# Performance work log

Measured on AMD Instinct MI355X. Metric: run time of the kernel, lower is better.

## Reference

```python
import jax, jax.numpy as jnp
import numpy as np

N = 50000   # nodes
E = 600000  # edges
D = 128     # in_feats
H = 128     # n_hidden
C = 47      # n_classes


def setup_inputs() -> dict:
    key = jax.random.key(0)
    ks = jax.random.split(key, 12)
    x = jax.random.normal(ks[0], (N, D), dtype=jnp.float32)
    src = jax.random.randint(ks[1], (E,), 0, N, dtype=jnp.int32)
    dst = jax.random.randint(ks[2], (E,), 0, N, dtype=jnp.int32)
    def lin(k, fi, fo):
        s = 1.0 / np.sqrt(fi)
        return jax.random.uniform(k, (fi, fo), jnp.float32, -s, s)
    return {
        "x": x, "src": src, "dst": dst,
        "W_self0": lin(ks[3], D, H), "W_neigh0": lin(ks[4], D, H), "b0": jnp.zeros((H,), jnp.float32),
        "W_self1": lin(ks[5], H, H), "W_neigh1": lin(ks[6], H, H), "b1": jnp.zeros((H,), jnp.float32),
        "W_self2": lin(ks[7], H, C), "W_neigh2": lin(ks[8], H, C), "b2": jnp.zeros((C,), jnp.float32),
    }


def _sage_layer(h, src, dst, W_self, W_neigh, b, act):
    # gather neighbor (src) features, mean-aggregate onto dst nodes
    msum = jax.ops.segment_sum(h[src], dst, num_segments=N)           # [N, F]
    deg = jax.ops.segment_sum(jnp.ones((src.shape[0], 1), h.dtype), dst, num_segments=N)
    h_neigh = msum / jnp.maximum(deg, 1.0)                            # zero-degree -> 0
    out = h @ W_self + h_neigh @ W_neigh + b
    return jax.nn.relu(out) if act else out


def reference(x, src, dst, W_self0, W_neigh0, b0, W_self1, W_neigh1, b1, W_self2, W_neigh2, b2):
    h = _sage_layer(x, src, dst, W_self0, W_neigh0, b0, True)
    h = _sage_layer(h, src, dst, W_self1, W_neigh1, b1, True)
    h = _sage_layer(h, src, dst, W_self2, W_neigh2, b2, False)
    return h
```

## Files before the change

kernel.cpp:

```cpp
#include <hip/hip_runtime.h>
#include <hip/hip_bf16.h>


#define THREADS 256

typedef unsigned short u16;
typedef __attribute__((ext_vector_type(8))) short bf16x8;
typedef __attribute__((ext_vector_type(4))) float f32x4;

__device__ inline u16 f2bf(float f) {
    union { float f; unsigned u; } v; v.f = f;
    unsigned r = (v.u + 0x7FFFu + ((v.u >> 16) & 1u)) >> 16;
    return (u16)r;
}
__device__ inline float bf2f(u16 b) {
    union { unsigned u; float f; } v; v.u = ((unsigned)b) << 16;
    return v.f;
}
__device__ inline unsigned pack2(float a, float b) {
    return (unsigned)f2bf(a) | ((unsigned)f2bf(b) << 16);
}

#define GLDS16(gp, lp)                                                         \
    __builtin_amdgcn_global_load_lds(                                          \
        (const __attribute__((address_space(1))) void*)(gp),                   \
        (__attribute__((address_space(3))) void*)(lp), 16, 0, 0)

__global__ void k_prepcount(const int* __restrict__ dst, int* __restrict__ deg, int E,
                            const float* __restrict__ x, u16* __restrict__ hi,
                            u16* __restrict__ lo, int n32,
                            const float* __restrict__ Ws0, const float* __restrict__ Wn0,
                            const float* __restrict__ Ws1, const float* __restrict__ Wn1,
                            const float* __restrict__ Ws2, const float* __restrict__ Wn2,
                            u16* __restrict__ Bt) {
    int idx = blockIdx.x * blockDim.x + threadIdx.x;
    if (idx < E) {
        atomicAdd(&deg[dst[idx]], 1);
        return;
    }
    idx -= E;
    if (idx < n32) {
        float4 v = ((const float4*)x)[idx];
        float h0 = bf2f(f2bf(v.x)), h1 = bf2f(f2bf(v.y));
        float h2 = bf2f(f2bf(v.z)), h3 = bf2f(f2bf(v.w));
        uint2 hp, lp;
        hp.x = pack2(h0, h1); hp.y = pack2(h2, h3);
        lp.x = pack2(v.x - h0, v.y - h1); lp.y = pack2(v.z - h2, v.w - h3);
        ((uint2*)hi)[idx] = hp;
        ((uint2*)lo)[idx] = lp;
        return;
    }
    idx -= n32;
    if (idx < 3 * 128 * 256) {
        int layer = idx >> 15;
        int within = idx & 32767;
        int col = within >> 8;
        int k = within & 255;
        const float* Ws = (layer == 0) ? Ws0 : (layer == 1) ? Ws1 : Ws2;
        const float* Wn = (layer == 0) ? Wn0 : (layer == 1) ? Wn1 : Wn2;
        int fo = (layer == 2) ? 47 : 128;
        float v = 0.f;
        if (col < fo) v = (k < 128) ? Ws[k * fo + col] : Wn[(k - 128) * fo + col];
        u16 h = f2bf(v);
        Bt[layer * 65536 + within] = h;
        Bt[layer * 65536 + 32768 + within] = f2bf(v - bf2f(h));
    }
}

__global__ void k_scan_block(const int* __restrict__ deg, int* __restrict__ off,
                             int* __restrict__ bsum, int n) {
    __shared__ int s[256];
    int t = threadIdx.x;
    int base = blockIdx.x * 1024 + t * 4;
    int v[4];
#pragma unroll
    for (int i = 0; i < 4; i++) v[i] = (base + i < n) ? deg[base + i] : 0;
    int sum = v[0] + v[1] + v[2] + v[3];
    int val = sum;
    s[t] = val;
    __syncthreads();
    for (int o = 1; o < 256; o <<= 1) {
        int x = (t >= o) ? s[t - o] : 0;
        __syncthreads();
        val += x;
        s[t] = val;
        __syncthreads();
    }
    int run = val - sum;
#pragma unroll
    for (int i = 0; i < 4; i++) {
        if (base + i < n) off[base + i] = run;
        run += v[i];
    }
    if (t == 255) bsum[blockIdx.x] = val;
}

__global__ void k_scan_bsum(int* __restrict__ bsum, int nb) {
    int lane = threadIdx.x;
    int carry = 0;
    for (int start = 0; start < nb; start += 64) {
        int i = start + lane;
        int orig = (i < nb) ? bsum[i] : 0;
        int v = orig;
#pragma unroll
        for (int o = 1; o < 64; o <<= 1) {
            int u = __shfl_up(v, o, 64);
            if (lane >= o) v += u;
        }
        if (i < nb) bsum[i] = carry + v - orig;
        carry += __shfl(v, 63, 64);
    }
}

__global__ void k_scan_add(int* __restrict__ off, const int* __restrict__ bsum, int n) {
    int t = threadIdx.x;
    int base = blockIdx.x * 1024 + t * 4;
    int add = bsum[blockIdx.x];
#pragma unroll
    for (int i = 0; i < 4; i++)
        if (base + i < n) off[base + i] += add;
}

__global__ void k_fill(const int* __restrict__ src, const int* __restrict__ dst,
                       const int* __restrict__ off, int* __restrict__ cur,
                       int* __restrict__ eidx, int E) {
    int e = blockIdx.x * blockDim.x + threadIdx.x;
    if (e < E) {
        int d = dst[e];
        int p = atomicAdd(&cur[d], 1);
        eidx[off[d] + p] = src[e];
    }
}

__global__ void k_aggregate(const u16* __restrict__ hi_in, const int* __restrict__ eidx,
                            const int* __restrict__ off, const int* __restrict__ deg,
                            u16* __restrict__ mhi, u16* __restrict__ mlo, int n) {
    int wv = blockIdx.x * 4 + (threadIdx.x >> 6);
    int lane = threadIdx.x & 63;
    int half = lane >> 5;
    int hl = lane & 31;
    int node = wv * 2 + half;
    if (node >= n) return;
    int cnt = deg[node];
    int base = off[node];
    const uint2* h2 = (const uint2*)hi_in;
    float4 acc = make_float4(0.f, 0.f, 0.f, 0.f);
    for (int j = 0; j < cnt; j += 8) {
        int s[8];
        float m[8];
#pragma unroll
        for (int u = 0; u < 8; u++) {
            int jj = j + u;
            s[u] = eidx[base + (jj < cnt ? jj : 0)];
            m[u] = (jj < cnt) ? 1.f : 0.f;
        }
        uint2 v[8];
#pragma unroll
        for (int u = 0; u < 8; u++) v[u] = h2[(size_t)s[u] * 32 + hl];
#pragma unroll
        for (int u = 0; u < 8; u++) {
            acc.x = fmaf(m[u], bf2f((u16)(v[u].x & 0xffffu)), acc.x);
            acc.y = fmaf(m[u], bf2f((u16)(v[u].x >> 16)), acc.y);
            acc.z = fmaf(m[u], bf2f((u16)(v[u].y & 0xffffu)), acc.z);
            acc.w = fmaf(m[u], bf2f((u16)(v[u].y >> 16)), acc.w);
        }
    }
    float iv = 1.0f / (float)(cnt > 1 ? cnt : 1);
    float a0 = acc.x * iv, a1 = acc.y * iv, a2 = acc.z * iv, a3 = acc.w * iv;
    float r0 = bf2f(f2bf(a0)), r1 = bf2f(f2bf(a1)), r2 = bf2f(f2bf(a2)), r3 = bf2f(f2bf(a3));
    uint2 hp, lp;
    hp.x = pack2(a0, a1); hp.y = pack2(a2, a3);
    lp.x = pack2(a0 - r0, a1 - r1); lp.y = pack2(a2 - r2, a3 - r3);
    ((uint2*)mhi)[(size_t)node * 32 + hl] = hp;
    ((uint2*)mlo)[(size_t)node * 32 + hl] = lp;
}

__global__ __launch_bounds__(256) void k_gemm_mfma(
    const u16* __restrict__ Ahi_s, const u16* __restrict__ Alo_s,
    const u16* __restrict__ Ahi_n, const u16* __restrict__ Alo_n,
    const u16* __restrict__ Bthi, const u16* __restrict__ Btlo,
    const float* __restrict__ bias, float* __restrict__ out_f32,
    u16* __restrict__ out_hi, u16* __restrict__ out_lo, int n, int fout, int relu) {
    __shared__ u16 sAhi[128 * 32];
    __shared__ u16 sAlo[128 * 32];
    __shared__ u16 sBhi[128 * 32];
    __shared__ u16 sBlo[128 * 32];

    int t = threadIdx.x;
    int w = t >> 6;
    int lane = t & 63;
    int wr = w >> 1, wc = w & 1;
    size_t row0 = (size_t)blockIdx.x * 128;

    f32x4 acc[4][4];
#pragma unroll
    for (int r = 0; r < 4; r++)
#pragma unroll
        for (int c = 0; c < 4; c++) acc[r][c] = (f32x4){0.f, 0.f, 0.f, 0.f};

    for (int kk = 0; kk < 256; kk += 32) {
        const u16* Phi = (kk < 128) ? Ahi_s : Ahi_n;
        const u16* Plo = (kk < 128) ? Alo_s : Alo_n;
        int kc = kk & 127;
        __syncthreads();
#pragma unroll
        for (int i = 0; i < 2; i++) {
            int r = w * 32 + i * 16 + (lane >> 2);
            int cb = (lane & 3) * 8;
            GLDS16(Phi + (row0 + r) * 128 + kc + cb, &sAhi[r * 32 + cb]);
            GLDS16(Plo + (row0 + r) * 128 + kc + cb, &sAlo[r * 32 + cb]);
        }
#pragma unroll
        for (int i = 0; i < 2; i++) {
            int c = w * 32 + i * 16 + (lane >> 2);
            int cb = (lane & 3) * 8;
            GLDS16(Bthi + (size_t)c * 256 + kk + cb, &sBhi[c * 32 + cb]);
            GLDS16(Btlo + (size_t)c * 256 + kk + cb, &sBlo[c * 32 + cb]);
        }
        __syncthreads();

        bf16x8 a_hi[4], a_lo[4], b_hi[4], b_lo[4];
        int q8 = (lane >> 4) * 8;
#pragma unroll
        for (int r = 0; r < 4; r++) {
            int ad = (wr * 64 + r * 16 + (lane & 15)) * 32 + q8;
            a_hi[r] = *(const bf16x8*)&sAhi[ad];
            a_lo[r] = *(const bf16x8*)&sAlo[ad];
        }
#pragma unroll
        for (int c = 0; c < 4; c++) {
            int ad = (wc * 64 + c * 16 + (lane & 15)) * 32 + q8;
            b_hi[c] = *(const bf16x8*)&sBhi[ad];
            b_lo[c] = *(const bf16x8*)&sBlo[ad];
        }
#pragma unroll
        for (int r = 0; r < 4; r++)
#pragma unroll
            for (int c = 0; c < 4; c++) {
                acc[r][c] = __builtin_amdgcn_mfma_f32_16x16x32_bf16(
                    a_hi[r], b_hi[c], acc[r][c], 0, 0, 0);
                acc[r][c] = __builtin_amdgcn_mfma_f32_16x16x32_bf16(
                    a_hi[r], b_lo[c], acc[r][c], 0, 0, 0);
                acc[r][c] = __builtin_amdgcn_mfma_f32_16x16x32_bf16(
                    a_lo[r], b_hi[c], acc[r][c], 0, 0, 0);
            }
    }

    int quad = lane >> 4;
    int lcol = lane & 15;
#pragma unroll
    for (int r = 0; r < 4; r++) {
#pragma unroll
        for (int c = 0; c < 4; c++) {
            int col = wc * 64 + c * 16 + lcol;
            float bv = (col < fout) ? bias[col] : 0.f;
#pragma unroll
            for (int g = 0; g < 4; g++) {
                size_t row = row0 + wr * 64 + r * 16 + quad * 4 + g;
                if (row >= (size_t)n || col >= fout) continue;
                float v = acc[r][c][g] + bv;
                if (relu) v = v > 0.f ? v : 0.f;
                if (out_f32) out_f32[row * fout + col] = v;
                if (out_hi) {
                    u16 h = f2bf(v);
                    out_hi[row * 128 + col] = h;
                    out_lo[row * 128 + col] = f2bf(v - bf2f(h));
                }
            }
        }
    }
}

extern "C" void kernel_launch(void* const* d_in, const int* in_sizes, int n_in,
                              void* d_out, int out_size, void* d_ws, size_t ws_size,
                              hipStream_t stream) {
    const float* x = (const float*)d_in[0];
    const int* src = (const int*)d_in[1];
    const int* dst = (const int*)d_in[2];
    const float* Ws0 = (const float*)d_in[3];
    const float* Wn0 = (const float*)d_in[4];
    const float* b0 = (const float*)d_in[5];
    const float* Ws1 = (const float*)d_in[6];
    const float* Wn1 = (const float*)d_in[7];
    const float* b1 = (const float*)d_in[8];
    const float* Ws2 = (const float*)d_in[9];
    const float* Wn2 = (const float*)d_in[10];
    const float* b2 = (const float*)d_in[11];
    float* out = (float*)d_out;

    const int N = in_sizes[0] / 128;
    const int E = in_sizes[1];
    const int Npad = ((N + 127) / 128) * 128;

    char* p = (char*)d_ws;
    u16* P0hi = (u16*)p; p += (size_t)Npad * 128 * 2;
    u16* P0lo = (u16*)p; p += (size_t)Npad * 128 * 2;
    u16* P1hi = (u16*)p; p += (size_t)Npad * 128 * 2;
    u16* P1lo = (u16*)p; p += (size_t)Npad * 128 * 2;
    u16* Mhi = (u16*)p; p += (size_t)Npad * 128 * 2;
    u16* Mlo = (u16*)p; p += (size_t)Npad * 128 * 2;
    u16* Bt = (u16*)p; p += 3 * 2 * 128 * 256 * 2;
    int* deg = (int*)p; p += (size_t)N * 4;
    int* cur = (int*)p; p += (size_t)N * 4;
    int* off = (int*)p; p += (size_t)N * 4;
    int* eidx = (int*)p; p += (size_t)E * 4;
    int* bsum = (int*)p;

    const int nbE = (E + THREADS - 1) / THREADS;
    const int nbScan = (N + 1023) / 1024;
    const int nbAgg = (N + 7) / 8;
    const int nbGemm = Npad / 128;
    const int prepTotal = E + N * 32 + 3 * 128 * 256;
    const int nbPrep = (prepTotal + THREADS - 1) / THREADS;

    hipMemsetAsync(deg, 0, (size_t)2 * N * sizeof(int), stream);

    k_prepcount<<<nbPrep, THREADS, 0, stream>>>(dst, deg, E, x, P0hi, P0lo, N * 32,
                                                Ws0, Wn0, Ws1, Wn1, Ws2, Wn2, Bt);
    k_scan_block<<<nbScan, 256, 0, stream>>>(deg, off, bsum, N);
    k_scan_bsum<<<1, 64, 0, stream>>>(bsum, nbScan);
    k_scan_add<<<nbScan, 256, 0, stream>>>(off, bsum, N);
    k_fill<<<nbE, THREADS, 0, stream>>>(src, dst, off, cur, eidx, E);

    k_aggregate<<<nbAgg, 256, 0, stream>>>(P0hi, eidx, off, deg, Mhi, Mlo, N);
    k_gemm_mfma<<<nbGemm, 256, 0, stream>>>(P0hi, P0lo, Mhi, Mlo,
                                            Bt + 0 * 65536, Bt + 0 * 65536 + 32768, b0,
                                            (float*)nullptr, P1hi, P1lo, N, 128, 1);
    k_aggregate<<<nbAgg, 256, 0, stream>>>(P1hi, eidx, off, deg, Mhi, Mlo, N);
    k_gemm_mfma<<<nbGemm, 256, 0, stream>>>(P1hi, P1lo, Mhi, Mlo,
                                            Bt + 1 * 65536, Bt + 1 * 65536 + 32768, b1,
                                            (float*)nullptr, P0hi, P0lo, N, 128, 1);
    k_aggregate<<<nbAgg, 256, 0, stream>>>(P0hi, eidx, off, deg, Mhi, Mlo, N);
    k_gemm_mfma<<<nbGemm, 256, 0, stream>>>(P0hi, P0lo, Mhi, Mlo,
                                            Bt + 2 * 65536, Bt + 2 * 65536 + 32768, b2,
                                            out, (u16*)nullptr, (u16*)nullptr, N, 47, 0);
}
```

Measured before the change: 317.1 us.

## Load GEMM operands directly from global into registers with smaller 64-row tiles

The MFMA GEMM no longer stages A and B tiles through shared memory with global_load_lds and barriers. Each wave now loads its bf16x8 fragments straight from global memory. The row tile shrinks from 128 to 64, which doubles the number of blocks and halves the accumulators per wave. This removes LDS traffic and synchronisation and raises parallelism, at the cost of redundant global/L2 reads of B and A across waves with no shared reuse.

```diff
diff --git a/kernel.cpp b/kernel.cpp
--- a/kernel.cpp
+++ b/kernel.cpp
@@ -20,11 +20,6 @@
 __device__ inline unsigned pack2(float a, float b) {
     return (unsigned)f2bf(a) | ((unsigned)f2bf(b) << 16);
 }
-
-#define GLDS16(gp, lp)                                                         \
-    __builtin_amdgcn_global_load_lds(                                          \
-        (const __attribute__((address_space(1))) void*)(gp),                   \
-        (__attribute__((address_space(3))) void*)(lp), 16, 0, 0)
 
 __global__ void k_prepcount(const int* __restrict__ dst, int* __restrict__ deg, int E,
                             const float* __restrict__ x, u16* __restrict__ hi,
@@ -181,60 +176,41 @@
     const u16* __restrict__ Bthi, const u16* __restrict__ Btlo,
     const float* __restrict__ bias, float* __restrict__ out_f32,
     u16* __restrict__ out_hi, u16* __restrict__ out_lo, int n, int fout, int relu) {
-    __shared__ u16 sAhi[128 * 32];
-    __shared__ u16 sAlo[128 * 32];
-    __shared__ u16 sBhi[128 * 32];
-    __shared__ u16 sBlo[128 * 32];
-
     int t = threadIdx.x;
     int w = t >> 6;
     int lane = t & 63;
     int wr = w >> 1, wc = w & 1;
-    size_t row0 = (size_t)blockIdx.x * 128;
-
-    f32x4 acc[4][4];
-#pragma unroll
-    for (int r = 0; r < 4; r++)
+    int m16 = lane & 15;
+    int q8 = (lane >> 4) * 8;
+    size_t row0 = (size_t)blockIdx.x * 64;
+
+    f32x4 acc[2][4];
+#pragma unroll
+    for (int r = 0; r < 2; r++)
 #pragma unroll
         for (int c = 0; c < 4; c++) acc[r][c] = (f32x4){0.f, 0.f, 0.f, 0.f};
 
+#pragma unroll
     for (int kk = 0; kk < 256; kk += 32) {
         const u16* Phi = (kk < 128) ? Ahi_s : Ahi_n;
         const u16* Plo = (kk < 128) ? Alo_s : Alo_n;
-        int kc = kk & 127;
-        __syncthreads();
-#pragma unroll
-        for (int i = 0; i < 2; i++) {
-            int r = w * 32 + i * 16 + (lane >> 2);
-            int cb = (lane & 3) * 8;
-            GLDS16(Phi + (row0 + r) * 128 + kc + cb, &sAhi[r * 32 + cb]);
-            GLDS16(Plo + (row0 + r) * 128 + kc + cb, &sAlo[r * 32 + cb]);
-        }
-#pragma unroll
-        for (int i = 0; i < 2; i++) {
-            int c = w * 32 + i * 16 + (lane >> 2);
-            int cb = (lane & 3) * 8;
-            GLDS16(Bthi + (size_t)c * 256 + kk + cb, &sBhi[c * 32 + cb]);
-            GLDS16(Btlo + (size_t)c * 256 + kk + cb, &sBlo[c * 32 + cb]);
-        }
-        __syncthreads();
-
-        bf16x8 a_hi[4], a_lo[4], b_hi[4], b_lo[4];
-        int q8 = (lane >> 4) * 8;
-#pragma unroll
-        for (int r = 0; r < 4; r++) {
-            int ad = (wr * 64 + r * 16 + (lane & 15)) * 32 + q8;
-            a_hi[r] = *(const bf16x8*)&sAhi[ad];
-            a_lo[r] = *(const bf16x8*)&sAlo[ad];
+        int kc = (kk & 127) + q8;
+
+        bf16x8 a_hi[2], a_lo[2], b_hi[4], b_lo[4];
+#pragma unroll
+        for (int r = 0; r < 2; r++) {
+            size_t ra = (row0 + wr * 32 + r * 16 + m16) * 128 + kc;
+            a_hi[r] = *(const bf16x8*)(Phi + ra);
+            a_lo[r] = *(const bf16x8*)(Plo + ra);
         }
 #pragma unroll
         for (int c = 0; c < 4; c++) {
-            int ad = (wc * 64 + c * 16 + (lane & 15)) * 32 + q8;
-            b_hi[c] = *(const bf16x8*)&sBhi[ad];
-            b_lo[c] = *(const bf16x8*)&sBlo[ad];
-        }
-#pragma unroll
-        for (int r = 0; r < 4; r++)
+            size_t ba = (size_t)(wc * 64 + c * 16 + m16) * 256 + kk + q8;
+            b_hi[c] = *(const bf16x8*)(Bthi + ba);
+            b_lo[c] = *(const bf16x8*)(Btlo + ba);
+        }
+#pragma unroll
+        for (int r = 0; r < 2; r++)
 #pragma unroll
             for (int c = 0; c < 4; c++) {
                 acc[r][c] = __builtin_amdgcn_mfma_f32_16x16x32_bf16(
@@ -249,14 +225,14 @@
     int quad = lane >> 4;
     int lcol = lane & 15;
 #pragma unroll
-    for (int r = 0; r < 4; r++) {
+    for (int r = 0; r < 2; r++) {
 #pragma unroll
         for (int c = 0; c < 4; c++) {
             int col = wc * 64 + c * 16 + lcol;
             float bv = (col < fout) ? bias[col] : 0.f;
 #pragma unroll
             for (int g = 0; g < 4; g++) {
-                size_t row = row0 + wr * 64 + r * 16 + quad * 4 + g;
+                size_t row = row0 + wr * 32 + r * 16 + quad * 4 + g;
                 if (row >= (size_t)n || col >= fout) continue;
                 float v = acc[r][c][g] + bv;
                 if (relu) v = v > 0.f ? v : 0.f;
@@ -290,7 +266,7 @@
 
     const int N = in_sizes[0] / 128;
     const int E = in_sizes[1];
-    const int Npad = ((N + 127) / 128) * 128;
+    const int Npad = ((N + 63) / 64) * 64;
 
     char* p = (char*)d_ws;
     u16* P0hi = (u16*)p; p += (size_t)Npad * 128 * 2;
@@ -309,7 +285,7 @@
     const int nbE = (E + THREADS - 1) / THREADS;
     const int nbScan = (N + 1023) / 1024;
     const int nbAgg = (N + 7) / 8;
-    const int nbGemm = Npad / 128;
+    const int nbGemm = Npad / 64;
     const int prepTotal = E + N * 32 + 3 * 128 * 256;
     const int nbPrep = (prepTotal + THREADS - 1) / THREADS;
 
```

Result: slower. 385.4 us (+21.5%).
